# Optimization experiments

Hardware: AMD Instinct MI355X
Metric: run time of the kernel (lower is better)

Reference implementation:

```python
import jax, jax.numpy as jnp
import numpy as np

DIM, DEPTH, DH, H, NLAT, MAXT, MAXF, FFM = 1024, 6, 64, 8, 64, 8, 16, 4
INNER = DH * H

def _ln(x, w, b, eps=1e-5):
    m = jnp.mean(x, axis=-1, keepdims=True)
    v = jnp.mean(jnp.square(x - m), axis=-1, keepdims=True)
    return (x - m) * jax.lax.rsqrt(v + eps) * w + b

def setup_inputs() -> dict:
    key = jax.random.key(0)
    ks = iter(jax.random.split(key, 32))
    s = 0.02
    d = {
        'x': jax.random.normal(next(ks), (2, 8, 16, 256, DIM), jnp.float32),
        'latents': jax.random.normal(next(ks), (NLAT, DIM), jnp.float32),
        'frame_emb': jax.random.normal(next(ks), (MAXF, DIM), jnp.float32),
        'media_emb': jax.random.normal(next(ks), (MAXT, 1, DIM), jnp.float32),
        'lnm_w': jnp.ones((DEPTH, DIM)), 'lnm_b': jnp.zeros((DEPTH, DIM)),
        'lnl_w': jnp.ones((DEPTH, DIM)), 'lnl_b': jnp.zeros((DEPTH, DIM)),
        'Wq': jax.random.normal(next(ks), (DEPTH, DIM, INNER), jnp.float32) * s,
        'Wkv': jax.random.normal(next(ks), (DEPTH, DIM, 2 * INNER), jnp.float32) * s,
        'Wo': jax.random.normal(next(ks), (DEPTH, INNER, DIM), jnp.float32) * s,
        'ffln_w': jnp.ones((DEPTH, DIM)), 'ffln_b': jnp.zeros((DEPTH, DIM)),
        'W1': jax.random.normal(next(ks), (DEPTH, DIM, FFM * DIM), jnp.float32) * s,
        'b1': jnp.zeros((DEPTH, FFM * DIM)),
        'W2': jax.random.normal(next(ks), (DEPTH, FFM * DIM, DIM), jnp.float32) * s,
        'b2': jnp.zeros((DEPTH, DIM)),
        'fln_w': jnp.ones((DIM,)), 'fln_b': jnp.zeros((DIM,)),
    }
    return d

def _split_heads(t):  # b T n (h d) -> b h T n d
    b, T, n, _ = t.shape
    return t.reshape(b, T, n, H, DH).transpose(0, 3, 1, 2, 4)

def _forward(x, latents, frame_emb, media_emb, lnm_w, lnm_b, lnl_w, lnl_b,
             Wq, Wkv, Wo, ffln_w, ffln_b, W1, b1, W2, b2, fln_w, fln_b):
    b, T, F, v, d = x.shape
    x = x + frame_emb[:F][None, None, :, None, :]      # b T F v d
    x = x.reshape(b, T, F * v, d)
    x = x + media_emb[:T]                              # [T,1,d] broadcasts
    lat = jnp.broadcast_to(latents, (b, T, NLAT, d))
    scale = DH ** -0.5
    for i in range(DEPTH):
        xn = _ln(x, lnm_w[i], lnm_b[i])
        ln_lat = _ln(lat, lnl_w[i], lnl_b[i])
        q = _split_heads(ln_lat @ Wq[i]) * scale       # b h T n2 dh
        kv = jnp.concatenate([xn, ln_lat], axis=2) @ Wkv[i]
        k, vv = jnp.split(kv, 2, axis=-1)
        k, vv = _split_heads(k), _split_heads(vv)      # b h T (n1+n2) dh
        sim = jnp.einsum('bhtid,bhtjd->bhtij', q, k)
        sim = sim - jax.lax.stop_gradient(jnp.max(sim, axis=-1, keepdims=True))
        attn = jax.nn.softmax(sim, axis=-1)
        o = jnp.einsum('bhtij,bhtjd->bhtid', attn, vv)
        o = o.transpose(0, 2, 3, 1, 4).reshape(b, T, NLAT, INNER)
        lat = (o @ Wo[i]) + lat
        h = _ln(lat, ffln_w[i], ffln_b[i])
        h = jax.nn.gelu(h @ W1[i] + b1[i], approximate=False) @ W2[i] + b2[i]
        lat = h + lat
    return _ln(lat, fln_w, fln_b)

def reference(x, latents, frame_emb, media_emb, lnm_w, lnm_b, lnl_w, lnl_b,
              Wq, Wkv, Wo, ffln_w, ffln_b, W1, b1, W2, b2, fln_w, fln_b):
    return _forward(x, latents, frame_emb, media_emb, lnm_w, lnm_b, lnl_w, lnl_b,
                    Wq, Wkv, Wo, ffln_w, ffln_b, W1, b1, W2, b2, fln_w, fln_b)
```

## Files before the change

### kernel.cpp

```cpp
#include <hip/hip_runtime.h>
#include <math.h>


#define DIM   1024
#define DEPTH 6
#define HEADS 8
#define NLAT  64
#define INNER 512
#define FFD   4096
#define XROWS 65536
#define LROWS 1024
#define NBT   16
#define QKVN  1536

typedef __attribute__((ext_vector_type(8))) short bf16x8;
typedef __attribute__((ext_vector_type(4))) float f32x4;

#define WAITV(n) asm volatile("s_waitcnt vmcnt(" #n ")" ::: "memory")

__device__ __forceinline__ short f2bf(float f) {
  union { float f; unsigned u; } v; v.f = f;
  unsigned r = v.u + 0x7fffu + ((v.u >> 16) & 1u);
  return (short)(r >> 16);
}

__device__ __forceinline__ void gload16(const void* g, void* l) {
  __builtin_amdgcn_global_load_lds(
      (const __attribute__((address_space(1))) unsigned int*)g,
      (__attribute__((address_space(3))) unsigned int*)l, 16, 0, 0);
}

__device__ __forceinline__ f32x4 zero_f4() { f32x4 z; z[0]=0.f; z[1]=0.f; z[2]=0.f; z[3]=0.f; return z; }
__device__ __forceinline__ bf16x8 zero_b8() { bf16x8 z;
#pragma unroll
  for (int e=0;e<8;e++) z[e]=0; return z; }

__device__ __forceinline__ void reduce2s(float& s, float& sq, float* sh) {
#pragma unroll
  for (int off = 32; off >= 1; off >>= 1) {
    s  += __shfl_xor(s,  off, 64);
    sq += __shfl_xor(sq, off, 64);
  }
  int t = threadIdx.x;
  if ((t & 63) == 0) { sh[(t >> 6)*2] = s; sh[(t >> 6)*2 + 1] = sq; }
  __syncthreads();
  s  = sh[0] + sh[2] + sh[4] + sh[6];
  sq = sh[1] + sh[3] + sh[5] + sh[7];
}

__global__ __launch_bounds__(256)
void mega0_kernel(const float* __restrict__ x, const float* __restrict__ fe,
                  const float* __restrict__ me, short* __restrict__ xhat,
                  const float* __restrict__ latents, const float* __restrict__ lnl_w,
                  const float* __restrict__ lnl_b, float* __restrict__ lat,
                  short* __restrict__ lnlat,
                  const float* __restrict__ Wkv, const float* __restrict__ Wq,
                  const float* __restrict__ Wo, const float* __restrict__ W1,
                  const float* __restrict__ W2, const float* __restrict__ lnm_w,
                  short* __restrict__ Wkvf_a, short* __restrict__ qkvW_a,
                  short* __restrict__ Wo_a, short* __restrict__ W1_a,
                  short* __restrict__ W2_a,
                  const float* __restrict__ lnm_b, float* __restrict__ kvb_part)
{
  __shared__ float smem[64*65];
  const int blk = blockIdx.x, t = threadIdx.x;

  if (blk < 16384) {
    int lane = t & 63;
    int r = blk*4 + (t >> 6);
    int f = (r >> 8) & 15, tt = (r >> 12) & 7;
    const float4* xp = (const float4*)(x + (size_t)r*DIM);
    const float4* fp = (const float4*)(fe + (size_t)f*DIM);
    const float4* mp = (const float4*)(me + (size_t)tt*DIM);
    float y[16];
    float s = 0.f, sq = 0.f;
#pragma unroll
    for (int k = 0; k < 4; k++) {
      float4 xv = xp[k*64 + lane], fv = fp[k*64 + lane], mv = mp[k*64 + lane];
      float a0 = xv.x+fv.x+mv.x, a1 = xv.y+fv.y+mv.y, a2 = xv.z+fv.z+mv.z, a3 = xv.w+fv.w+mv.w;
      y[k*4+0]=a0; y[k*4+1]=a1; y[k*4+2]=a2; y[k*4+3]=a3;
      s += a0+a1+a2+a3; sq += a0*a0+a1*a1+a2*a2+a3*a3;
    }
#pragma unroll
    for (int off = 32; off >= 1; off >>= 1) {
      s  += __shfl_xor(s,  off, 64);
      sq += __shfl_xor(sq, off, 64);
    }
    float mean = s * (1.0f/DIM);
    float var  = sq * (1.0f/DIM) - mean*mean;
    float rs = rsqrtf(var + 1e-5f);
    short4* op = (short4*)(xhat + (size_t)r*DIM);
#pragma unroll
    for (int k = 0; k < 4; k++) {
      short4 o;
      o.x = f2bf((y[k*4+0]-mean)*rs); o.y = f2bf((y[k*4+1]-mean)*rs);
      o.z = f2bf((y[k*4+2]-mean)*rs); o.w = f2bf((y[k*4+3]-mean)*rs);
      op[k*64 + lane] = o;
    }
  } else if (blk < 17408) {
    int r = blk - 16384;
    int i = r & 63;
    float4 a = ((const float4*)(latents + (size_t)i*DIM))[t];
    ((float4*)(lat + (size_t)r*DIM))[t] = a;
    float s = a.x+a.y+a.z+a.w;
    float sq = a.x*a.x+a.y*a.y+a.z*a.z+a.w*a.w;
    reduce2s(s, sq, smem);
    float mean = s*(1.0f/DIM), var = sq*(1.0f/DIM) - mean*mean;
    float rs = rsqrtf(var + 1e-5f);
    float4 wv = ((const float4*)lnl_w)[t], bv = ((const float4*)lnl_b)[t];
    short4 o;
    o.x = f2bf((a.x-mean)*rs*wv.x + bv.x);
    o.y = f2bf((a.y-mean)*rs*wv.y + bv.y);
    o.z = f2bf((a.z-mean)*rs*wv.z + bv.z);
    o.w = f2bf((a.w-mean)*rs*wv.w + bv.w);
    ((short4*)(lnlat + (size_t)r*DIM))[t] = o;
  } else if (blk < 34304) {
    int bb = blk - 17408;
    int L = bb / 2816;
    int b = bb % 2816;
    const float* lWkv = Wkv + (size_t)L*DIM*DIM;
    const float* src; short* dst; const float* fold = nullptr; float scale = 1.0f;
    int K, N, bx, ntx;
    if (b < 256)      { src=lWkv; dst=Wkvf_a + (size_t)L*DIM*DIM; fold=lnm_w + (size_t)L*DIM; K=1024; N=1024; bx=b; ntx=16; }
    else if (b < 384) { src=Wq + (size_t)L*DIM*INNER; dst=qkvW_a + (size_t)L*QKVN*DIM; scale=0.125f; K=1024; N=512; bx=b-256; ntx=8; }
    else if (b < 640) { src=lWkv; dst=qkvW_a + (size_t)L*QKVN*DIM + (size_t)512*1024; K=1024; N=1024; bx=b-384; ntx=16; }
    else if (b < 768) { src=Wo + (size_t)L*INNER*DIM; dst=Wo_a + (size_t)L*INNER*DIM; K=512;  N=1024; bx=b-640; ntx=16; }
    else if (b < 1792){ src=W1 + (size_t)L*DIM*FFD; dst=W1_a + (size_t)L*DIM*FFD; K=1024; N=4096; bx=b-768; ntx=64; }
    else              { src=W2 + (size_t)L*FFD*DIM; dst=W2_a + (size_t)L*FFD*DIM; K=4096; N=1024; bx=b-1792; ntx=16; }
    int n0 = (bx % ntx)*64, k0 = (bx / ntx)*64;
#pragma unroll
    for (int i = 0; i < 16; i++) {
      int rr = (t >> 6) + i*4, cc = t & 63;
      float v = src[(size_t)(k0+rr)*N + n0 + cc] * scale;
      if (fold) v *= fold[k0 + rr];
      smem[rr*65 + cc] = v;
    }
    __syncthreads();
#pragma unroll
    for (int i = 0; i < 16; i++) {
      int nn = (t >> 6) + i*4, kk = t & 63;
      dst[(size_t)(n0+nn)*K + k0 + kk] = f2bf(smem[kk*65 + nn]);
    }
  } else {
    int b2 = blk - 34304;
    int z = b2 & 15, i = b2 >> 4;
    const float* W = Wkv + (size_t)i*DIM*DIM;
    const float* bv = lnm_b + (size_t)i*DIM;
    float acc0=0,acc1=0,acc2=0,acc3=0;
    for (int k = z*64; k < z*64+64; k++) {
      float b3 = bv[k];
      const float* Wr = W + (size_t)k*DIM;
      acc0 += b3 * Wr[t];       acc1 += b3 * Wr[t+256];
      acc2 += b3 * Wr[t+512];   acc3 += b3 * Wr[t+768];
    }
    float* o = kvb_part + (size_t)(i*16 + z)*DIM;
    o[t] = acc0; o[t+256] = acc1; o[t+512] = acc2; o[t+768] = acc3;
  }
}

__global__ __launch_bounds__(256)
void kvbred_kernel(const float* __restrict__ kvb_part, float* __restrict__ kvb)
{
  int i = blockIdx.x, t = threadIdx.x;
#pragma unroll
  for (int j = 0; j < 4; j++) {
    int col = t + j*256;
    float s = 0.f;
#pragma unroll
    for (int z = 0; z < 16; z++) s += kvb_part[(size_t)(i*16 + z)*DIM + col];
    kvb[i*DIM + col] = s;
  }
}


__device__ __forceinline__ void kv256_path(
    const short* __restrict__ A, const short* __restrict__ Bt,
    short* __restrict__ C, const float* __restrict__ bias, int id, char* ldsc)
{
  const int t = threadIdx.x, lane = t & 63, wid = t >> 6;
  const int wm = wid >> 2, wn = wid & 3;
  const int K = DIM, N = DIM;

  const int work = (id & 7) * 128 + (id >> 3);
  const int bn = work & 3, bm = work >> 2;
  const int m0 = bm * 256, n0 = bn * 256;

  f32x4 acc[8][4];
#pragma unroll
  for (int m=0;m<8;m++)
#pragma unroll
    for (int n=0;n<4;n++) acc[m][n] = zero_f4();

  const int hK = K << 7;
  const short* pA[2]; const short* pB[2]; int ldst[2];
#pragma unroll
  for (int i = 0; i < 2; i++) {
    int chunk = i*512 + t;
    int rh = chunk >> 3, sl = chunk & 7;
    int ss = sl ^ (rh & 7);
    pA[i] = A + (size_t)(m0 + rh)*K + ss*8;
    pB[i] = Bt + (size_t)(n0 + rh)*K + ss*8;
    ldst[i] = (i*512 + (wid << 6))*16;
  }
  auto stage = [&](int tile, int mat, int half) {
    char* dbase = ldsc + mat*65536 + (tile & 1)*32768 + half*16384;
#pragma unroll
    for (int i = 0; i < 2; i++) {
      const short* src = (mat ? pB[i] : pA[i]) + half*hK + tile*64;
      gload16(src, dbase + ldst[i]);
    }
  };

  const int sk0 = (((lane >> 4)    ) ^ (lane & 7)) * 16;
  const int sk1 = ((4 + (lane >> 4)) ^ (lane & 7)) * 16;
  const int rowb = (lane & 15) * 128;
  const char* aB[2] = { ldsc + wm*16384 + rowb + sk0, ldsc + wm*16384 + rowb + sk1 };
  const char* bB[2] = { ldsc + 65536 + wn*8192 + rowb + sk0, ldsc + 65536 + wn*8192 + rowb + sk1 };

#define PHASE(BUF, Q, STAGE_STMT, GATE) do {                               \
    if ((Q) == 0) {                                                        \
      _Pragma("unroll") for (int n_=0;n_<4;n_++)                           \
        _Pragma("unroll") for (int k_=0;k_<2;k_++)                         \
          bfr[n_][k_] = *(const bf16x8*)(bB[k_] + (BUF)*32768 + n_*2048);  \
    }                                                                      \
    _Pragma("unroll") for (int i_=0;i_<2;i_++)                             \
      _Pragma("unroll") for (int k_=0;k_<2;k_++)                           \
        afr[i_][k_] = *(const bf16x8*)(aB[k_] + (BUF)*32768 + (2*(Q)+i_)*2048); \
    STAGE_STMT;                                                            \
    GATE;                                                                  \
    __builtin_amdgcn_sched_barrier(0);                                     \
    __builtin_amdgcn_s_barrier();                                          \
    asm volatile("s_waitcnt lgkmcnt(0)" ::: "memory");                     \
    __builtin_amdgcn_sched_barrier(0);                                     \
    __builtin_amdgcn_s_setprio(1);                                         \
    _Pragma("unroll") for (int k_=0;k_<2;k_++)                             \
      _Pragma("unroll") for (int i_=0;i_<2;i_++)                           \
        _Pragma("unroll") for (int n_=0;n_<4;n_++)                         \
          acc[2*(Q)+i_][n_] = __builtin_amdgcn_mfma_f32_16x16x32_bf16(     \
              afr[i_][k_], bfr[n_][k_], acc[2*(Q)+i_][n_], 0, 0, 0);       \
    __builtin_amdgcn_s_setprio(0);                                         \
    __builtin_amdgcn_sched_barrier(0);                                     \
    __builtin_amdgcn_s_barrier();                                          \
  } while (0)

  const int NU = K >> 7;
  stage(0, 0, 0); stage(0, 0, 1); stage(0, 1, 0); stage(0, 1, 1);
  stage(1, 1, 0); stage(1, 1, 1);
  WAITV(4);
  __builtin_amdgcn_sched_barrier(0);
  __builtin_amdgcn_s_barrier();

#pragma unroll 1
  for (int u = 0; u < NU; ++u) {
    const int t0 = 2*u, t1 = t0 + 1;
    const bool more = (u + 1 < NU);
    bf16x8 bfr[4][2], afr[2][2];
    PHASE(0, 0, stage(t1, 0, 0),               (void)0);
    PHASE(0, 1, stage(t1, 0, 1),               (void)0);
    PHASE(0, 2, if (more) stage(t0+2, 1, 0),   (void)0);
    PHASE(0, 3, if (more) stage(t0+2, 1, 1),   if (more) { WAITV(4); } else { WAITV(0); });
    PHASE(1, 0, if (more) stage(t0+2, 0, 0),   (void)0);
    PHASE(1, 1, if (more) stage(t0+2, 0, 1),   (void)0);
    PHASE(1, 2, if (more) stage(t1+2, 1, 0),   (void)0);
    PHASE(1, 3, if (more) stage(t1+2, 1, 1),   if (more) { WAITV(4); });
  }
#undef PHASE

  const int g = lane >> 4;
#pragma unroll
  for (int m=0;m<8;m++) {
#pragma unroll
    for (int n=0;n<4;n++) {
#pragma unroll
      for (int r=0;r<4;r++) {
        int mm = m0 + wm*128 + m*16 + g*4 + r;
        int nn = n0 + wn*64 + n*16 + (lane & 15);
        float v = acc[m][n][r] + bias[nn];
        C[(size_t)mm*N + nn] = f2bf(v);
      }
    }
  }
}

__device__ __forceinline__ void qkv_path(
    const short* __restrict__ A, const short* __restrict__ Bt,
    short* __restrict__ C, int q, char* ldsc)
{
  const int t = threadIdx.x, lane = t & 63, wid = t >> 6;
  const int m0 = (q & 7) * 128, n0 = (q >> 3) * 128;
  const int wr = (wid >> 2) * 64, wc = (wid & 3) * 32;
  char* As = ldsc;
  char* Bs = ldsc + 16384;

  f32x4 acc[4][2];
#pragma unroll
  for (int i=0;i<4;i++)
#pragma unroll
    for (int j=0;j<2;j++) acc[i][j] = zero_f4();

  for (int kt = 0; kt < DIM; kt += 64) {
#pragma unroll
    for (int i = 0; i < 2; i++) {
      int chunk = i*512 + t;
      int row = chunk >> 3, slot = chunk & 7;
      int ss = slot ^ (row & 7);
      gload16(A + (size_t)(m0 + row)*DIM + kt + ss*8, As + (i*512 + (wid<<6))*16);
    }
#pragma unroll
    for (int i = 0; i < 2; i++) {
      int chunk = i*512 + t;
      int row = chunk >> 3, slot = chunk & 7;
      int ss = slot ^ (row & 7);
      gload16(Bt + (size_t)(n0 + row)*DIM + kt + ss*8, Bs + (i*512 + (wid<<6))*16);
    }
    __syncthreads();
#pragma unroll
    for (int ks = 0; ks < 2; ks++) {
      bf16x8 af[4], bfr[2];
#pragma unroll
      for (int i=0;i<4;i++) {
        int row = wr + i*16 + (lane & 15);
        int slot = (ks*4 + (lane >> 4)) ^ (row & 7);
        af[i] = *(const bf16x8*)(As + row*128 + slot*16);
      }
#pragma unroll
      for (int j=0;j<2;j++) {
        int row = wc + j*16 + (lane & 15);
        int slot = (ks*4 + (lane >> 4)) ^ (row & 7);
        bfr[j] = *(const bf16x8*)(Bs + row*128 + slot*16);
      }
#pragma unroll
      for (int i=0;i<4;i++)
#pragma unroll
        for (int j=0;j<2;j++)
          acc[i][j] = __builtin_amdgcn_mfma_f32_16x16x32_bf16(af[i], bfr[j], acc[i][j], 0, 0, 0);
    }
    __syncthreads();
  }

  const int g = lane >> 4;
#pragma unroll
  for (int i=0;i<4;i++) {
#pragma unroll
    for (int j=0;j<2;j++) {
#pragma unroll
      for (int r=0;r<4;r++) {
        int mm = m0 + wr + i*16 + g*4 + r;
        int nn = n0 + wc + j*16 + (lane & 15);
        C[(size_t)mm*QKVN + nn] = f2bf(acc[i][j][r]);
      }
    }
  }
}

__global__ __launch_bounds__(512, 1)
void mega1_kernel(const short* __restrict__ xhat, const short* __restrict__ Wkvf,
                  const float* __restrict__ kvb_i, short* __restrict__ kvbuf,
                  const short* __restrict__ lnlat, const short* __restrict__ qkvW,
                  short* __restrict__ qkvlat)
{
  __shared__ __align__(16) short lds[65536];
  int b = blockIdx.x;
  if (b < 1024) kv256_path(xhat, Wkvf, kvbuf, kvb_i, b, (char*)lds);
  else          qkv_path(lnlat, qkvW, qkvlat, b - 1024, (char*)lds);
}

template<int EPI, bool HAS_BIAS>
__global__ __launch_bounds__(256, 2)
void gemm_kernel(const short* __restrict__ A, const short* __restrict__ Bt,
                 void* __restrict__ Cout, const float* __restrict__ bias,
                 int M, int N, int K, int ldk)
{
  __shared__ __align__(16) short As[128*64];
  __shared__ __align__(16) short Bs[128*64];
  const int t = threadIdx.x;
  const int lane = t & 63, w = t >> 6;
  const int m0 = blockIdx.x * 128, n0 = blockIdx.y * 128;
  const int wr = (w >> 1) * 64, wc = (w & 1) * 64;
  const short* Ap = A + (size_t)blockIdx.z * K;
  const short* Btp = Bt + (size_t)blockIdx.z * K;

  f32x4 acc[4][4];
#pragma unroll
  for (int i=0;i<4;i++)
#pragma unroll
    for (int j=0;j<4;j++) acc[i][j] = zero_f4();

  for (int kt = 0; kt < K; kt += 64) {
#pragma unroll
    for (int i = 0; i < 4; i++) {
      int chunk = i*256 + t;
      int row = chunk >> 3, slot = chunk & 7;
      int ss = slot ^ (row & 7);
      gload16(Ap + (size_t)(m0 + row)*ldk + kt + ss*8,
              (char*)As + (i*256 + (w<<6))*16);
    }
#pragma unroll
    for (int i = 0; i < 4; i++) {
      int chunk = i*256 + t;
      int row = chunk >> 3, slot = chunk & 7;
      int ss = slot ^ (row & 7);
      gload16(Btp + (size_t)(n0 + row)*ldk + kt + ss*8,
              (char*)Bs + (i*256 + (w<<6))*16);
    }
    __syncthreads();

#pragma unroll
    for (int ks = 0; ks < 2; ks++) {
      bf16x8 af[4], bfr[4];
#pragma unroll
      for (int i=0;i<4;i++) {
        int row = wr + i*16 + (lane & 15);
        int slot = (ks*4 + (lane >> 4)) ^ (row & 7);
        af[i] = *(const bf16x8*)((const char*)As + row*128 + slot*16);
        int nrow = wc + i*16 + (lane & 15);
        int nslot = (ks*4 + (lane >> 4)) ^ (nrow & 7);
        bfr[i] = *(const bf16x8*)((const char*)Bs + nrow*128 + nslot*16);
      }
#pragma unroll
      for (int i=0;i<4;i++)
#pragma unroll
        for (int j=0;j<4;j++)
          acc[i][j] = __builtin_amdgcn_mfma_f32_16x16x32_bf16(af[i], bfr[j], acc[i][j], 0, 0, 0);
    }
    __syncthreads();
  }

  const int g = lane >> 4;
#pragma unroll
  for (int i=0;i<4;i++) {
#pragma unroll
    for (int j=0;j<4;j++) {
#pragma unroll
      for (int r=0;r<4;r++) {
        int m = m0 + wr + i*16 + g*4 + r;
        int n = n0 + wc + j*16 + (lane & 15);
        float v = acc[i][j][r];
        if (EPI == 1) {
          if (HAS_BIAS) v += bias[n];
          float gl = 0.5f * v * (1.0f + erff(v * 0.70710678f));
          ((short*)Cout)[(size_t)m*N + n] = f2bf(gl);
        } else {
          ((float*)Cout)[(size_t)blockIdx.z*M*N + (size_t)m*N + n] = v;
        }
      }
    }
  }
}

__global__ __launch_bounds__(256)
void wored_ffln_kernel(const float* __restrict__ part, float* __restrict__ lat,
                       const float* __restrict__ w, const float* __restrict__ bb,
                       short* __restrict__ hbuf)
{
  __shared__ float sh[8];
  int r = blockIdx.x, t = threadIdx.x;
  int idx = r*256 + t;
  float4 a = ((float4*)lat)[idx];
#pragma unroll
  for (int z = 0; z < 4; z++) {
    float4 p = ((const float4*)(part + (size_t)z*LROWS*DIM))[idx];
    a.x += p.x; a.y += p.y; a.z += p.z; a.w += p.w;
  }
  ((float4*)lat)[idx] = a;
  float s = a.x+a.y+a.z+a.w;
  float sq = a.x*a.x+a.y*a.y+a.z*a.z+a.w*a.w;
  reduce2s(s, sq, sh);
  float mean = s*(1.0f/DIM), var = sq*(1.0f/DIM) - mean*mean;
  float rs = rsqrtf(var + 1e-5f);
  float4 wv = ((const float4*)w)[t], bv = ((const float4*)bb)[t];
  short4 o;
  o.x = f2bf((a.x-mean)*rs*wv.x + bv.x);
  o.y = f2bf((a.y-mean)*rs*wv.y + bv.y);
  o.z = f2bf((a.z-mean)*rs*wv.z + bv.z);
  o.w = f2bf((a.w-mean)*rs*wv.w + bv.w);
  ((short4*)(hbuf + (size_t)r*DIM))[t] = o;
}

template<bool LAST>
__global__ __launch_bounds__(256)
void w2red_ln_kernel(const float* __restrict__ part, const float* __restrict__ b2,
                     float* __restrict__ lat, const float* __restrict__ w,
                     const float* __restrict__ bb, void* __restrict__ dst)
{
  __shared__ float sh[8];
  int r = blockIdx.x, t = threadIdx.x;
  int idx = r*256 + t;
  float4 a = ((float4*)lat)[idx];
  float4 b4 = ((const float4*)b2)[t];
  a.x += b4.x; a.y += b4.y; a.z += b4.z; a.w += b4.w;
#pragma unroll
  for (int z = 0; z < 4; z++) {
    float4 p = ((const float4*)(part + (size_t)z*LROWS*DIM))[idx];
    a.x += p.x; a.y += p.y; a.z += p.z; a.w += p.w;
  }
  ((float4*)lat)[idx] = a;
  float s = a.x+a.y+a.z+a.w;
  float sq = a.x*a.x+a.y*a.y+a.z*a.z+a.w*a.w;
  reduce2s(s, sq, sh);
  float mean = s*(1.0f/DIM), var = sq*(1.0f/DIM) - mean*mean;
  float rs = rsqrtf(var + 1e-5f);
  float4 wv = ((const float4*)w)[t], bv = ((const float4*)bb)[t];
  float o0 = (a.x-mean)*rs*wv.x + bv.x;
  float o1 = (a.y-mean)*rs*wv.y + bv.y;
  float o2 = (a.z-mean)*rs*wv.z + bv.z;
  float o3 = (a.w-mean)*rs*wv.w + bv.w;
  if (LAST) {
    float4 o; o.x=o0; o.y=o1; o.z=o2; o.w=o3;
    ((float4*)((float*)dst + (size_t)r*DIM))[t] = o;
  } else {
    short4 o; o.x=f2bf(o0); o.y=f2bf(o1); o.z=f2bf(o2); o.w=f2bf(o3);
    ((short4*)((short*)dst + (size_t)r*DIM))[t] = o;
  }
}

__global__ __launch_bounds__(256, 2)
void attn_part_kernel(const short* __restrict__ qkvlat, const short* __restrict__ kvbuf,
                      float* __restrict__ part_O, float* __restrict__ part_m,
                      float* __restrict__ part_l)
{
  __shared__ __align__(16) short q_sh[64*64];
  __shared__ __align__(16) short K_sh[128*64];
  __shared__ __align__(16) short VT_sh[64*128];
  __shared__ __align__(16) short P_sh[64*132];

  const int t = threadIdx.x, lane = t & 63, w = t >> 6;
  const int bid = blockIdx.x;
  const int s = bid & 3, bh = bid >> 2;
  const int h = bh & 7, bt = bh >> 3;

  {
    const short* qsrc = qkvlat + (size_t)(bt*64)*QKVN + h*64;
#pragma unroll
    for (int i = 0; i < 2; i++) {
      int chunk = i*256 + t;
      int row = chunk >> 3, slot = chunk & 7;
      gload16(qsrc + (size_t)row*QKVN + ((slot ^ (row & 7))*8),
              (char*)q_sh + (i*256 + (w<<6))*16);
    }
  }

  float m_run[4], l_run[4];
#pragma unroll
  for (int r=0;r<4;r++){ m_run[r] = -1e30f; l_run[r] = 0.f; }
  f32x4 oacc[4];
#pragma unroll
  for (int j=0;j<4;j++) oacc[j] = zero_f4();

  const int nch = (s == 3) ? 9 : 8;
  for (int c5 = 0; c5 < nch; c5++) {
    __syncthreads();
    const bool isLat = (c5 == 8);
    const int jv = isLat ? 4 : 8;
    const short* kbase; int kstride, valid;
    if (!isLat) {
      kbase = kvbuf + ((size_t)bt*4096 + (s*8 + c5)*128)*DIM + h*64;
      kstride = DIM; valid = 128;
    } else {
      kbase = qkvlat + (size_t)(bt*64)*QKVN + 512 + h*64;
      kstride = QKVN; valid = 64;
    }
    const short* vbase = kbase + 512;

#pragma unroll
    for (int i = 0; i < 4; i++) {
      int chunk = i*256 + t;
      int row = chunk >> 3, slot = chunk & 7;
      gload16(kbase + (size_t)row*kstride + ((slot ^ (row & 7))*8),
              (char*)K_sh + (i*256 + (w<<6))*16);
    }
#pragma unroll
    for (int i = 0; i < 4; i++) {
      int c = i*256 + t;
      int row = c >> 3, slot = c & 7;
      bf16x8 v = (row < valid) ? *(const bf16x8*)(vbase + (size_t)row*kstride + slot*8) : zero_b8();
#pragma unroll
      for (int e=0;e<8;e++) {
        int dh = slot*8 + e;
        VT_sh[dh*128 + ((row + (dh & 0x78)) & 127)] = v[e];
      }
    }
    __syncthreads();

    f32x4 sacc[8];
#pragma unroll
    for (int j=0;j<8;j++) sacc[j] = zero_f4();
#pragma unroll
    for (int ks=0; ks<2; ks++) {
      int arow = w*16 + (lane & 15);
      int aslot = (ks*4 + (lane >> 4)) ^ (arow & 7);
      bf16x8 af = *(const bf16x8*)((const char*)q_sh + arow*128 + aslot*16);
#pragma unroll
      for (int j=0;j<8;j++) {
        int brow = j*16 + (lane & 15);
        int bslot = (ks*4 + (lane >> 4)) ^ (brow & 7);
        bf16x8 bv = *(const bf16x8*)((const char*)K_sh + brow*128 + bslot*16);
        sacc[j] = __builtin_amdgcn_mfma_f32_16x16x32_bf16(af, bv, sacc[j], 0, 0, 0);
      }
    }

    float mx[4];
#pragma unroll
    for (int r=0;r<4;r++) mx[r] = -1e30f;
#pragma unroll
    for (int j=0;j<8;j++) {
      if (j < jv) {
#pragma unroll
        for (int r=0;r<4;r++) mx[r] = fmaxf(mx[r], sacc[j][r]);
      }
    }
#pragma unroll
    for (int m2=1; m2<16; m2<<=1) {
#pragma unroll
      for (int r=0;r<4;r++) mx[r] = fmaxf(mx[r], __shfl_xor(mx[r], m2, 64));
    }
    float alpha[4], rowsum[4];
#pragma unroll
    for (int r=0;r<4;r++) {
      float nm = fmaxf(m_run[r], mx[r]);
      alpha[r] = __expf(m_run[r] - nm);
      m_run[r] = nm;
      rowsum[r] = 0.f;
    }
#pragma unroll
    for (int j=0;j<8;j++) {
#pragma unroll
      for (int r=0;r<4;r++) {
        float p = 0.f;
        if (j < jv) { p = __expf(sacc[j][r] - m_run[r]); rowsum[r] += p; }
        P_sh[(w*16 + (lane>>4)*4 + r)*132 + j*16 + (lane & 15)] = f2bf(p);
      }
    }
#pragma unroll
    for (int m2=1; m2<16; m2<<=1) {
#pragma unroll
      for (int r=0;r<4;r++) rowsum[r] += __shfl_xor(rowsum[r], m2, 64);
    }
#pragma unroll
    for (int r=0;r<4;r++) l_run[r] = l_run[r]*alpha[r] + rowsum[r];
#pragma unroll
    for (int j=0;j<4;j++) {
#pragma unroll
      for (int r=0;r<4;r++) oacc[j][r] *= alpha[r];
    }
    __syncthreads();

#pragma unroll
    for (int ks=0; ks<4; ks++) {
      int prow = w*16 + (lane & 15);
      bf16x8 af = *(const bf16x8*)((const char*)P_sh + prow*264 + ks*64 + (lane >> 4)*16);
#pragma unroll
      for (int j=0;j<4;j++) {
        int dh = j*16 + (lane & 15);
        int kb = (ks*4 + (lane >> 4))*8;
        const short* vp = VT_sh + dh*128 + ((kb + (dh & 0x78)) & 127);
        bf16x8 bv = *(const bf16x8*)vp;
        oacc[j] = __builtin_amdgcn_mfma_f32_16x16x32_bf16(af, bv, oacc[j], 0, 0, 0);
      }
    }
  }

  {
    float* Ob = part_O + (size_t)bid*4096;
    int rbase = w*16 + (lane>>4)*4;
#pragma unroll
    for (int j=0;j<4;j++) {
#pragma unroll
      for (int r=0;r<4;r++)
        Ob[(rbase + r)*64 + j*16 + (lane & 15)] = oacc[j][r];
    }
    if ((lane & 15) == 0) {
#pragma unroll
      for (int r=0;r<4;r++) {
        part_m[(size_t)bid*64 + rbase + r] = m_run[r];
        part_l[(size_t)bid*64 + rbase + r] = l_run[r];
      }
    }
  }
}

__global__ __launch_bounds__(256)
void attn_combine_kernel(const float* __restrict__ part_O, const float* __restrict__ part_m,
                         const float* __restrict__ part_l, short* __restrict__ obuf)
{
  int bh = blockIdx.x, t = threadIdx.x;
  int q = t >> 2, c0 = (t & 3) * 16;
  int bt = bh >> 3, h = bh & 7;
  float m4[4], w4[4];
  float mmax = -1e30f;
#pragma unroll
  for (int s=0;s<4;s++) { m4[s] = part_m[(size_t)(bh*4+s)*64 + q]; mmax = fmaxf(mmax, m4[s]); }
  float lt = 0.f;
#pragma unroll
  for (int s=0;s<4;s++) { w4[s] = __expf(m4[s] - mmax); lt += w4[s] * part_l[(size_t)(bh*4+s)*64 + q]; }
  float inv = 1.0f / lt;
  float4 acc[4];
#pragma unroll
  for (int u=0;u<4;u++) { acc[u].x=0.f; acc[u].y=0.f; acc[u].z=0.f; acc[u].w=0.f; }
#pragma unroll
  for (int s=0;s<4;s++) {
    const float4* Ob = (const float4*)(part_O + ((size_t)(bh*4+s)*64 + q)*64 + c0);
#pragma unroll
    for (int u=0;u<4;u++) {
      float4 v = Ob[u];
      acc[u].x += w4[s]*v.x; acc[u].y += w4[s]*v.y;
      acc[u].z += w4[s]*v.z; acc[u].w += w4[s]*v.w;
    }
  }
  short* ob = obuf + (size_t)(bt*64 + q)*INNER + h*64 + c0;
#pragma unroll
  for (int u=0;u<4;u++) {
    short4 o;
    o.x = f2bf(acc[u].x*inv); o.y = f2bf(acc[u].y*inv);
    o.z = f2bf(acc[u].z*inv); o.w = f2bf(acc[u].w*inv);
    ((short4*)ob)[u] = o;
  }
}

extern "C" void kernel_launch(void* const* d_in, const int* in_sizes, int n_in,
                              void* d_out, int out_size, void* d_ws, size_t ws_size,
                              hipStream_t stream)
{
  (void)in_sizes; (void)n_in; (void)out_size; (void)ws_size;
  const float* x        = (const float*)d_in[0];
  const float* latents  = (const float*)d_in[1];
  const float* frame_e  = (const float*)d_in[2];
  const float* media_e  = (const float*)d_in[3];
  const float* lnm_w    = (const float*)d_in[4];
  const float* lnm_b    = (const float*)d_in[5];
  const float* lnl_w    = (const float*)d_in[6];
  const float* lnl_b    = (const float*)d_in[7];
  const float* Wq       = (const float*)d_in[8];
  const float* Wkv      = (const float*)d_in[9];
  const float* Wo       = (const float*)d_in[10];
  const float* ffln_w   = (const float*)d_in[11];
  const float* ffln_b   = (const float*)d_in[12];
  const float* W1       = (const float*)d_in[13];
  const float* b1       = (const float*)d_in[14];
  const float* W2       = (const float*)d_in[15];
  const float* b2       = (const float*)d_in[16];
  const float* fln_w    = (const float*)d_in[17];
  const float* fln_b    = (const float*)d_in[18];
  float* out = (float*)d_out;

  char* ws = (char*)d_ws;
  size_t off = 0;
  short* xhat   = (short*)(ws + off); off += (size_t)XROWS*DIM*2;
  short* kvbuf  = (short*)(ws + off); off += (size_t)XROWS*DIM*2;
  short* Wkvf_a = (short*)(ws + off); off += (size_t)DEPTH*DIM*DIM*2;
  short* qkvW_a = (short*)(ws + off); off += (size_t)DEPTH*QKVN*DIM*2;
  short* Wo_a   = (short*)(ws + off); off += (size_t)DEPTH*INNER*DIM*2;
  short* W1_a   = (short*)(ws + off); off += (size_t)DEPTH*DIM*FFD*2;
  short* W2_a   = (short*)(ws + off); off += (size_t)DEPTH*FFD*DIM*2;
  float* kvb    = (float*)(ws + off); off += (size_t)DEPTH*DIM*4;
  float* kvbp   = (float*)(ws + off); off += (size_t)DEPTH*16*DIM*4;
  float* lat    = (float*)(ws + off); off += (size_t)LROWS*DIM*4;
  short* lnlat  = (short*)(ws + off); off += (size_t)LROWS*DIM*2;
  short* qkvlat = (short*)(ws + off); off += (size_t)LROWS*QKVN*2;
  short* obuf   = (short*)(ws + off); off += (size_t)LROWS*INNER*2;
  short* hbuf   = (short*)(ws + off); off += (size_t)LROWS*DIM*2;
  short* h1     = (short*)(ws + off); off += (size_t)LROWS*FFD*2;
  float* wopart = (float*)(ws + off); off += (size_t)4*LROWS*DIM*4;
  float* part_O = (float*)(ws + off); off += (size_t)4*LROWS*DIM*4;
  float* w2part = part_O;
  float* part_m = (float*)(ws + off); off += (size_t)512*64*4;
  float* part_l = (float*)(ws + off); off += (size_t)512*64*4;

  mega0_kernel<<<34400, 256, 0, stream>>>(
      x, frame_e, media_e, xhat,
      latents, lnl_w, lnl_b, lat, lnlat,
      Wkv, Wq, Wo, W1, W2, lnm_w,
      Wkvf_a, qkvW_a, Wo_a, W1_a, W2_a,
      lnm_b, kvbp);
  kvbred_kernel<<<DEPTH, 256, 0, stream>>>(kvbp, kvb);

  for (int i = 0; i < DEPTH; i++) {
    const short* Wkv_f = Wkvf_a + (size_t)i*DIM*DIM;
    const short* qkvW  = qkvW_a + (size_t)i*QKVN*DIM;
    const short* Wo_h  = Wo_a   + (size_t)i*INNER*DIM;
    const short* W1_h  = W1_a   + (size_t)i*DIM*FFD;
    const short* W2_h  = W2_a   + (size_t)i*FFD*DIM;

    mega1_kernel<<<1120, 512, 0, stream>>>(
        xhat, Wkv_f, kvb + i*DIM, kvbuf, lnlat, qkvW, qkvlat);
    attn_part_kernel<<<512, 256, 0, stream>>>(qkvlat, kvbuf, part_O, part_m, part_l);
    attn_combine_kernel<<<128, 256, 0, stream>>>(part_O, part_m, part_l, obuf);
    gemm_kernel<4,false><<<dim3(LROWS/128, DIM/128, 4), 256, 0, stream>>>(
        obuf, Wo_h, wopart, nullptr, LROWS, DIM, 128, INNER);
    wored_ffln_kernel<<<LROWS, 256, 0, stream>>>(
        wopart, lat, ffln_w + i*DIM, ffln_b + i*DIM, hbuf);
    gemm_kernel<1,true><<<dim3(LROWS/128, FFD/128), 256, 0, stream>>>(
        hbuf, W1_h, h1, b1 + (size_t)i*FFD, LROWS, FFD, DIM, DIM);
    gemm_kernel<4,false><<<dim3(LROWS/128, DIM/128, 4), 256, 0, stream>>>(
        h1, W2_h, w2part, nullptr, LROWS, DIM, DIM, FFD);
    if (i < DEPTH-1)
      w2red_ln_kernel<false><<<LROWS, 256, 0, stream>>>(
          w2part, b2 + (size_t)i*DIM, lat, lnl_w + (i+1)*DIM, lnl_b + (i+1)*DIM, lnlat);
    else
      w2red_ln_kernel<true><<<LROWS, 256, 0, stream>>>(
          w2part, b2 + (size_t)i*DIM, lat, fln_w, fln_b, out);
  }
}
```

Before: 1.892 ms.

## Fuse attention split-combine into Wo GEMM and split prep kernel

The attention combine step, which merges the four partial softmax results, now runs inside a new Wo GEMM kernel. It builds the bf16 A tile directly in LDS from part_O/part_m/part_l, so the separate combine launch and the obuf round trip are gone. The big setup kernel is also split into a dedicated x-normalization kernel and a weight-prep kernel. The cost is that each of the 8 N-tile blocks recomputes the same combine work for its rows, so part_O is read redundantly.

```diff
diff --git a/kernel.cpp b/kernel.cpp
--- a/kernel.cpp
+++ b/kernel.cpp
@@ -49,56 +49,59 @@
 }
 
 __global__ __launch_bounds__(256)
-void mega0_kernel(const float* __restrict__ x, const float* __restrict__ fe,
-                  const float* __restrict__ me, short* __restrict__ xhat,
-                  const float* __restrict__ latents, const float* __restrict__ lnl_w,
-                  const float* __restrict__ lnl_b, float* __restrict__ lat,
-                  short* __restrict__ lnlat,
-                  const float* __restrict__ Wkv, const float* __restrict__ Wq,
-                  const float* __restrict__ Wo, const float* __restrict__ W1,
-                  const float* __restrict__ W2, const float* __restrict__ lnm_w,
-                  short* __restrict__ Wkvf_a, short* __restrict__ qkvW_a,
-                  short* __restrict__ Wo_a, short* __restrict__ W1_a,
-                  short* __restrict__ W2_a,
-                  const float* __restrict__ lnm_b, float* __restrict__ kvb_part)
+void prep_kernel(const float* __restrict__ x, const float* __restrict__ fe,
+                 const float* __restrict__ me, short* __restrict__ xhat)
+{
+  int lane = threadIdx.x & 63;
+  int r = blockIdx.x*4 + (threadIdx.x >> 6);
+  int f = (r >> 8) & 15, tt = (r >> 12) & 7;
+  const float4* xp = (const float4*)(x + (size_t)r*DIM);
+  const float4* fp = (const float4*)(fe + (size_t)f*DIM);
+  const float4* mp = (const float4*)(me + (size_t)tt*DIM);
+  float y[16];
+  float s = 0.f, sq = 0.f;
+#pragma unroll
+  for (int k = 0; k < 4; k++) {
+    float4 xv = xp[k*64 + lane], fv = fp[k*64 + lane], mv = mp[k*64 + lane];
+    float a0 = xv.x+fv.x+mv.x, a1 = xv.y+fv.y+mv.y, a2 = xv.z+fv.z+mv.z, a3 = xv.w+fv.w+mv.w;
+    y[k*4+0]=a0; y[k*4+1]=a1; y[k*4+2]=a2; y[k*4+3]=a3;
+    s += a0+a1+a2+a3; sq += a0*a0+a1*a1+a2*a2+a3*a3;
+  }
+#pragma unroll
+  for (int off = 32; off >= 1; off >>= 1) {
+    s  += __shfl_xor(s,  off, 64);
+    sq += __shfl_xor(sq, off, 64);
+  }
+  float mean = s * (1.0f/DIM);
+  float var  = sq * (1.0f/DIM) - mean*mean;
+  float rs = rsqrtf(var + 1e-5f);
+  short4* op = (short4*)(xhat + (size_t)r*DIM);
+#pragma unroll
+  for (int k = 0; k < 4; k++) {
+    short4 o;
+    o.x = f2bf((y[k*4+0]-mean)*rs); o.y = f2bf((y[k*4+1]-mean)*rs);
+    o.z = f2bf((y[k*4+2]-mean)*rs); o.w = f2bf((y[k*4+3]-mean)*rs);
+    op[k*64 + lane] = o;
+  }
+}
+
+__global__ __launch_bounds__(256)
+void mega0b_kernel(const float* __restrict__ latents, const float* __restrict__ lnl_w,
+                   const float* __restrict__ lnl_b, float* __restrict__ lat,
+                   short* __restrict__ lnlat,
+                   const float* __restrict__ Wkv, const float* __restrict__ Wq,
+                   const float* __restrict__ Wo, const float* __restrict__ W1,
+                   const float* __restrict__ W2, const float* __restrict__ lnm_w,
+                   short* __restrict__ Wkvf_a, short* __restrict__ qkvW_a,
+                   short* __restrict__ Wo_a, short* __restrict__ W1_a,
+                   short* __restrict__ W2_a,
+                   const float* __restrict__ lnm_b, float* __restrict__ kvb_part)
 {
   __shared__ float smem[64*65];
   const int blk = blockIdx.x, t = threadIdx.x;
 
-  if (blk < 16384) {
-    int lane = t & 63;
-    int r = blk*4 + (t >> 6);
-    int f = (r >> 8) & 15, tt = (r >> 12) & 7;
-    const float4* xp = (const float4*)(x + (size_t)r*DIM);
-    const float4* fp = (const float4*)(fe + (size_t)f*DIM);
-    const float4* mp = (const float4*)(me + (size_t)tt*DIM);
-    float y[16];
-    float s = 0.f, sq = 0.f;
-#pragma unroll
-    for (int k = 0; k < 4; k++) {
-      float4 xv = xp[k*64 + lane], fv = fp[k*64 + lane], mv = mp[k*64 + lane];
-      float a0 = xv.x+fv.x+mv.x, a1 = xv.y+fv.y+mv.y, a2 = xv.z+fv.z+mv.z, a3 = xv.w+fv.w+mv.w;
-      y[k*4+0]=a0; y[k*4+1]=a1; y[k*4+2]=a2; y[k*4+3]=a3;
-      s += a0+a1+a2+a3; sq += a0*a0+a1*a1+a2*a2+a3*a3;
-    }
-#pragma unroll
-    for (int off = 32; off >= 1; off >>= 1) {
-      s  += __shfl_xor(s,  off, 64);
-      sq += __shfl_xor(sq, off, 64);
-    }
-    float mean = s * (1.0f/DIM);
-    float var  = sq * (1.0f/DIM) - mean*mean;
-    float rs = rsqrtf(var + 1e-5f);
-    short4* op = (short4*)(xhat + (size_t)r*DIM);
-#pragma unroll
-    for (int k = 0; k < 4; k++) {
-      short4 o;
-      o.x = f2bf((y[k*4+0]-mean)*rs); o.y = f2bf((y[k*4+1]-mean)*rs);
-      o.z = f2bf((y[k*4+2]-mean)*rs); o.w = f2bf((y[k*4+3]-mean)*rs);
-      op[k*64 + lane] = o;
-    }
-  } else if (blk < 17408) {
-    int r = blk - 16384;
+  if (blk < 1024) {
+    int r = blk;
     int i = r & 63;
     float4 a = ((const float4*)(latents + (size_t)i*DIM))[t];
     ((float4*)(lat + (size_t)r*DIM))[t] = a;
@@ -114,8 +117,8 @@
     o.z = f2bf((a.z-mean)*rs*wv.z + bv.z);
     o.w = f2bf((a.w-mean)*rs*wv.w + bv.w);
     ((short4*)(lnlat + (size_t)r*DIM))[t] = o;
-  } else if (blk < 34304) {
-    int bb = blk - 17408;
+  } else if (blk < 17920) {
+    int bb = blk - 1024;
     int L = bb / 2816;
     int b = bb % 2816;
     const float* lWkv = Wkv + (size_t)L*DIM*DIM;
@@ -142,7 +145,7 @@
       dst[(size_t)(n0+nn)*K + k0 + kk] = f2bf(smem[kk*65 + nn]);
     }
   } else {
-    int b2 = blk - 34304;
+    int b2 = blk - 17920;
     int z = b2 & 15, i = b2 >> 4;
     const float* W = Wkv + (size_t)i*DIM*DIM;
     const float* bv = lnm_b + (size_t)i*DIM;
@@ -171,7 +174,6 @@
     kvb[i*DIM + col] = s;
   }
 }
-
 
 __device__ __forceinline__ void kv256_path(
     const short* __restrict__ A, const short* __restrict__ Bt,
@@ -448,6 +450,103 @@
   }
 }
 
+__global__ __launch_bounds__(256, 2)
+void woattn_kernel(const float* __restrict__ part_O, const float* __restrict__ part_m,
+                   const float* __restrict__ part_l, const short* __restrict__ Bt,
+                   float* __restrict__ Cout)
+{
+  __shared__ __align__(16) short As[128*64];
+  __shared__ __align__(16) short Bs[128*64];
+  const int t = threadIdx.x, lane = t & 63, w = t >> 6;
+  const int m0 = blockIdx.x * 128, n0 = blockIdx.y * 128, z = blockIdx.z;
+  const int wr = (w >> 1) * 64, wc = (w & 1) * 64;
+
+  f32x4 acc[4][4];
+#pragma unroll
+  for (int i=0;i<4;i++)
+#pragma unroll
+    for (int j=0;j<4;j++) acc[i][j] = zero_f4();
+
+#pragma unroll 1
+  for (int kt2 = 0; kt2 < 2; kt2++) {
+    const int h = z*2 + kt2;
+#pragma unroll
+    for (int i = 0; i < 4; i++) {
+      int chunk = i*256 + t;
+      int row = chunk >> 3, slot = chunk & 7;
+      int m = m0 + row;
+      int bt = m >> 6, q = m & 63;
+      int bh4 = (bt*8 + h)*4;
+      float m4[4];
+      float mmax = -1e30f;
+#pragma unroll
+      for (int s=0;s<4;s++){ m4[s] = part_m[(size_t)(bh4+s)*64 + q]; mmax = fmaxf(mmax, m4[s]); }
+      float w4[4]; float lt = 0.f;
+#pragma unroll
+      for (int s=0;s<4;s++){ w4[s] = __expf(m4[s]-mmax); lt += w4[s]*part_l[(size_t)(bh4+s)*64 + q]; }
+      float inv = 1.0f/lt;
+      float a8[8];
+#pragma unroll
+      for (int e=0;e<8;e++) a8[e] = 0.f;
+#pragma unroll
+      for (int s=0;s<4;s++){
+        const float4* p = (const float4*)(part_O + ((size_t)(bh4+s)*64 + q)*64 + slot*8);
+        float4 p0 = p[0], p1 = p[1];
+        float ws = w4[s];
+        a8[0]+=ws*p0.x; a8[1]+=ws*p0.y; a8[2]+=ws*p0.z; a8[3]+=ws*p0.w;
+        a8[4]+=ws*p1.x; a8[5]+=ws*p1.y; a8[6]+=ws*p1.z; a8[7]+=ws*p1.w;
+      }
+      bf16x8 v;
+#pragma unroll
+      for (int e=0;e<8;e++) v[e] = f2bf(a8[e]*inv);
+      *(bf16x8*)((char*)As + row*128 + ((slot ^ (row & 7))*16)) = v;
+    }
+#pragma unroll
+    for (int i = 0; i < 4; i++) {
+      int chunk = i*256 + t;
+      int row = chunk >> 3, slot = chunk & 7;
+      int ss = slot ^ (row & 7);
+      gload16(Bt + (size_t)(n0 + row)*INNER + h*64 + ss*8,
+              (char*)Bs + (i*256 + (w<<6))*16);
+    }
+    __syncthreads();
+
+#pragma unroll
+    for (int ks = 0; ks < 2; ks++) {
+      bf16x8 af[4], bfr[4];
+#pragma unroll
+      for (int i=0;i<4;i++) {
+        int row = wr + i*16 + (lane & 15);
+        int slot = (ks*4 + (lane >> 4)) ^ (row & 7);
+        af[i] = *(const bf16x8*)((const char*)As + row*128 + slot*16);
+        int nrow = wc + i*16 + (lane & 15);
+        int nslot = (ks*4 + (lane >> 4)) ^ (nrow & 7);
+        bfr[i] = *(const bf16x8*)((const char*)Bs + nrow*128 + nslot*16);
+      }
+#pragma unroll
+      for (int i=0;i<4;i++)
+#pragma unroll
+        for (int j=0;j<4;j++)
+          acc[i][j] = __builtin_amdgcn_mfma_f32_16x16x32_bf16(af[i], bfr[j], acc[i][j], 0, 0, 0);
+    }
+    __syncthreads();
+  }
+
+  const int g = lane >> 4;
+#pragma unroll
+  for (int i=0;i<4;i++) {
+#pragma unroll
+    for (int j=0;j<4;j++) {
+#pragma unroll
+      for (int r=0;r<4;r++) {
+        int m = m0 + wr + i*16 + g*4 + r;
+        int n = n0 + wc + j*16 + (lane & 15);
+        Cout[(size_t)blockIdx.z*LROWS*DIM + (size_t)m*DIM + n] = acc[i][j][r];
+      }
+    }
+  }
+}
+
 __global__ __launch_bounds__(256)
 void wored_ffln_kernel(const float* __restrict__ part, float* __restrict__ lat,
                        const float* __restrict__ w, const float* __restrict__ bb,
@@ -676,44 +775,6 @@
         part_l[(size_t)bid*64 + rbase + r] = l_run[r];
       }
     }
-  }
-}
-
-__global__ __launch_bounds__(256)
-void attn_combine_kernel(const float* __restrict__ part_O, const float* __restrict__ part_m,
-                         const float* __restrict__ part_l, short* __restrict__ obuf)
-{
-  int bh = blockIdx.x, t = threadIdx.x;
-  int q = t >> 2, c0 = (t & 3) * 16;
-  int bt = bh >> 3, h = bh & 7;
-  float m4[4], w4[4];
-  float mmax = -1e30f;
-#pragma unroll
-  for (int s=0;s<4;s++) { m4[s] = part_m[(size_t)(bh*4+s)*64 + q]; mmax = fmaxf(mmax, m4[s]); }
-  float lt = 0.f;
-#pragma unroll
-  for (int s=0;s<4;s++) { w4[s] = __expf(m4[s] - mmax); lt += w4[s] * part_l[(size_t)(bh*4+s)*64 + q]; }
-  float inv = 1.0f / lt;
-  float4 acc[4];
-#pragma unroll
-  for (int u=0;u<4;u++) { acc[u].x=0.f; acc[u].y=0.f; acc[u].z=0.f; acc[u].w=0.f; }
-#pragma unroll
-  for (int s=0;s<4;s++) {
-    const float4* Ob = (const float4*)(part_O + ((size_t)(bh*4+s)*64 + q)*64 + c0);
-#pragma unroll
-    for (int u=0;u<4;u++) {
-      float4 v = Ob[u];
-      acc[u].x += w4[s]*v.x; acc[u].y += w4[s]*v.y;
-      acc[u].z += w4[s]*v.z; acc[u].w += w4[s]*v.w;
-    }
-  }
-  short* ob = obuf + (size_t)(bt*64 + q)*INNER + h*64 + c0;
-#pragma unroll
-  for (int u=0;u<4;u++) {
-    short4 o;
-    o.x = f2bf(acc[u].x*inv); o.y = f2bf(acc[u].y*inv);
-    o.z = f2bf(acc[u].z*inv); o.w = f2bf(acc[u].w*inv);
-    ((short4*)ob)[u] = o;
   }
 }
 
@@ -757,7 +818,6 @@
   float* lat    = (float*)(ws + off); off += (size_t)LROWS*DIM*4;
   short* lnlat  = (short*)(ws + off); off += (size_t)LROWS*DIM*2;
   short* qkvlat = (short*)(ws + off); off += (size_t)LROWS*QKVN*2;
-  short* obuf   = (short*)(ws + off); off += (size_t)LROWS*INNER*2;
   short* hbuf   = (short*)(ws + off); off += (size_t)LROWS*DIM*2;
   short* h1     = (short*)(ws + off); off += (size_t)LROWS*FFD*2;
   float* wopart = (float*)(ws + off); off += (size_t)4*LROWS*DIM*4;
@@ -766,8 +826,8 @@
   float* part_m = (float*)(ws + off); off += (size_t)512*64*4;
   float* part_l = (float*)(ws + off); off += (size_t)512*64*4;
 
-  mega0_kernel<<<34400, 256, 0, stream>>>(
-      x, frame_e, media_e, xhat,
+  prep_kernel<<<XROWS/4, 256, 0, stream>>>(x, frame_e, media_e, xhat);
+  mega0b_kernel<<<18016, 256, 0, stream>>>(
       latents, lnl_w, lnl_b, lat, lnlat,
       Wkv, Wq, Wo, W1, W2, lnm_w,
       Wkvf_a, qkvW_a, Wo_a, W1_a, W2_a,
@@ -784,9 +844,8 @@
     mega1_kernel<<<1120, 512, 0, stream>>>(
         xhat, Wkv_f, kvb + i*DIM, kvbuf, lnlat, qkvW, qkvlat);
     attn_part_kernel<<<512, 256, 0, stream>>>(qkvlat, kvbuf, part_O, part_m, part_l);
-    attn_combine_kernel<<<128, 256, 0, stream>>>(part_O, part_m, part_l, obuf);
-    gemm_kernel<4,false><<<dim3(LROWS/128, DIM/128, 4), 256, 0, stream>>>(
-        obuf, Wo_h, wopart, nullptr, LROWS, DIM, 128, INNER);
+    woattn_kernel<<<dim3(8, 8, 4), 256, 0, stream>>>(
+        part_O, part_m, part_l, Wo_h, wopart);
     wored_ffln_kernel<<<LROWS, 256, 0, stream>>>(
         wopart, lat, ffln_w + i*DIM, ffln_b + i*DIM, hbuf);
     gemm_kernel<1,true><<<dim3(LROWS/128, FFD/128), 256, 0, stream>>>(
```

After: 1.935 ms. +2.3%, slower.
